# Kernel optimization log

Hardware: AMD Instinct MI355X
Metric: run time of the kernel (lower is better)

The kernel has to match this reference:

```python
import jax, jax.numpy as jnp
import numpy as np

B, L1, NUM_C, DIM_S, SIZE_M = 64, 199, 1000, 64, 50


def setup_inputs() -> dict:
    key = jax.random.key(0)
    ks = jax.random.split(key, 16)
    inp = {
        "cseqs": jax.random.randint(ks[0], (B, L1), 0, NUM_C),
        "rseqs": jax.random.randint(ks[1], (B, L1), 0, 2),
        "shft_cseqs": jax.random.randint(ks[2], (B, L1), 0, NUM_C),
        "shft_rseqs": jax.random.randint(ks[3], (B, L1), 0, 2),
        # learned parameters (linear weights stored as [in, out])
        "kemb": jax.random.normal(ks[4], (NUM_C, DIM_S)) * 0.05,
        "vemb": jax.random.normal(ks[5], (2 * NUM_C, DIM_S)) * 0.05,
        "Mk": jax.random.normal(ks[6], (SIZE_M, DIM_S)) * (2.0 / DIM_S) ** 0.5,
        "Mv0": jax.random.normal(ks[7], (SIZE_M, DIM_S)) * (2.0 / DIM_S) ** 0.5,
        "Wf": jax.random.normal(ks[8], (2 * DIM_S, DIM_S)) * 0.05,
        "bf": jnp.zeros((DIM_S,)),
        "We": jax.random.normal(ks[9], (DIM_S, DIM_S)) * 0.05,
        "be": jnp.zeros((DIM_S,)),
        "Wa": jax.random.normal(ks[10], (DIM_S, DIM_S)) * 0.05,
        "ba": jnp.zeros((DIM_S,)),
        "Wp": jax.random.normal(ks[11], (DIM_S, 1)) * 0.05,
        "bp": jnp.zeros((1,)),
    }
    return inp


def reference(cseqs, rseqs, shft_cseqs, shft_rseqs,
              kemb, vemb, Mk, Mv0, Wf, bf, We, be, Wa, ba, Wp, bp):
    # reconstruct full-length sequences: [B, L] with L = L1 + 1
    q = jnp.concatenate([cseqs[:, :1], shft_cseqs], axis=-1)
    r = jnp.concatenate([rseqs[:, :1], shft_rseqs], axis=-1)
    x = q + NUM_C * r

    k = kemb[q]                                  # [B, L, D]
    v = vemb[x]                                  # [B, L, D]

    w = jax.nn.softmax(k @ Mk.T, axis=-1)        # [B, L, M] correlation weights
    e = jax.nn.sigmoid(v @ We + be)              # [B, L, D] erase
    a = jnp.tanh(v @ Wa + ba)                    # [B, L, D] add

    def step(Mvt, inp):
        et, at, wt = inp                         # [B,D], [B,D], [B,M]
        Mv_prev = Mvt                            # memory BEFORE this update (used for read)
        Mvt = Mvt * (1.0 - wt[:, :, None] * et[:, None, :]) + wt[:, :, None] * at[:, None, :]
        return Mvt, Mv_prev

    Mv_init = jnp.broadcast_to(Mv0[None], (B, SIZE_M, DIM_S))
    _, Mv_prev = jax.lax.scan(
        step, Mv_init,
        (e.transpose(1, 0, 2), a.transpose(1, 0, 2), w.transpose(1, 0, 2)))
    Mv_prev = Mv_prev.transpose(1, 0, 2, 3)      # [B, L, M, D]

    read = jnp.einsum('blm,blmd->bld', w, Mv_prev)   # weighted read
    info = jnp.concatenate([read, k], axis=-1)       # [B, L, 2D]
    f = jnp.tanh(info @ Wf + bf)                     # dropout is identity in eval
    p = jax.nn.sigmoid((f @ Wp + bp).squeeze(-1))    # [B, L]
    return p
```

## Files before the change

kernel.cpp:

```cpp
#include <hip/hip_runtime.h>
#include <math.h>

#define B    64
#define L1   199
#define L    200
#define NC   1000
#define D    64
#define M    50
#define SEG  4
#define TS   50
#define WV   5
#define MPW  10
#define BLK  320

__global__ __launch_bounds__(64) void phase0(
    const float* __restrict__ kemb, const float* __restrict__ vemb,
    const float* __restrict__ Mk,
    const float* __restrict__ We, const float* __restrict__ be,
    const float* __restrict__ Wa, const float* __restrict__ ba,
    const float* __restrict__ Wf,
    float* __restrict__ wtab, float* __restrict__ etab,
    float* __restrict__ atab, float* __restrict__ ktab)
{
    __shared__ __align__(16) float lrow[4 * D];
    const int lane = threadIdx.x;
    const int bid  = blockIdx.x;

    if (bid < 250) {
        const int r0 = bid * 4;
        #pragma unroll
        for (int i = 0; i < 4; ++i)
            lrow[i * D + lane] = kemb[(size_t)(r0 + i) * D + lane];
        __syncthreads();

        float Mk_r[D];
        {
            const int mrow = (lane < M) ? lane : (M - 1);
            #pragma unroll
            for (int d = 0; d < D; d += 4) {
                const float4 t4 = *(const float4*)(Mk + mrow * D + d);
                Mk_r[d] = t4.x; Mk_r[d+1] = t4.y; Mk_r[d+2] = t4.z; Mk_r[d+3] = t4.w;
            }
        }
        #pragma unroll
        for (int i = 0; i < 4; ++i) {
            float c0 = 0.f, c1 = 0.f;
            #pragma unroll
            for (int d = 0; d < D; d += 4) {
                const float4 kb = *(const float4*)&lrow[i * D + d];
                c0 = fmaf(Mk_r[d],     kb.x, c0);
                c1 = fmaf(Mk_r[d + 1], kb.y, c1);
                c0 = fmaf(Mk_r[d + 2], kb.z, c0);
                c1 = fmaf(Mk_r[d + 3], kb.w, c1);
            }
            const float logit = (lane < M) ? (c0 + c1) : -INFINITY;
            float mx = logit;
            #pragma unroll
            for (int off = 32; off; off >>= 1) mx = fmaxf(mx, __shfl_xor(mx, off, 64));
            const float ex = expf(logit - mx);
            float sm = ex;
            #pragma unroll
            for (int off = 32; off; off >>= 1) sm += __shfl_xor(sm, off, 64);
            if (lane < M) wtab[(size_t)(r0 + i) * M + lane] = ex / sm;
        }
    } else if (bid < 1250) {
        const bool is_e = (bid < 750);
        const int  r0   = (is_e ? (bid - 250) : (bid - 750)) * 4;
        #pragma unroll
        for (int i = 0; i < 4; ++i)
            lrow[i * D + lane] = vemb[(size_t)(r0 + i) * D + lane];
        __syncthreads();

        const float* __restrict__ W   = is_e ? We : Wa;
        float*       __restrict__ dst = is_e ? etab : atab;
        float Wc[D];
        #pragma unroll
        for (int din = 0; din < D; ++din) Wc[din] = W[din * D + lane];
        const float br = is_e ? be[lane] : ba[lane];

        #pragma unroll
        for (int i = 0; i < 4; ++i) {
            float c0 = 0.f, c1 = 0.f;
            #pragma unroll
            for (int d = 0; d < D; d += 4) {
                const float4 vb = *(const float4*)&lrow[i * D + d];
                c0 = fmaf(Wc[d],     vb.x, c0);
                c1 = fmaf(Wc[d + 1], vb.y, c1);
                c0 = fmaf(Wc[d + 2], vb.z, c0);
                c1 = fmaf(Wc[d + 3], vb.w, c1);
            }
            const float acc = c0 + c1;
            const float r = is_e ? (1.f / (1.f + expf(-(acc + br))))
                                 : tanhf(acc + br);
            dst[(size_t)(r0 + i) * D + lane] = r;
        }
    } else {
        const int r0 = (bid - 1250) * 4;
        #pragma unroll
        for (int i = 0; i < 4; ++i)
            lrow[i * D + lane] = kemb[(size_t)(r0 + i) * D + lane];
        __syncthreads();

        float Wc[D];
        #pragma unroll
        for (int i = 0; i < D; ++i) Wc[i] = Wf[(size_t)(D + i) * D + lane];

        #pragma unroll
        for (int i = 0; i < 4; ++i) {
            float f1 = 0.f;
            #pragma unroll
            for (int d = 0; d < D; d += 4) {
                const float4 kb = *(const float4*)&lrow[i * D + d];
                f1 = fmaf(Wc[d],     kb.x, f1);
                f1 = fmaf(Wc[d + 1], kb.y, f1);
                f1 = fmaf(Wc[d + 2], kb.z, f1);
                f1 = fmaf(Wc[d + 3], kb.w, f1);
            }
            ktab[(size_t)(r0 + i) * D + lane] = f1;
        }
    }
}

__global__ __launch_bounds__(BLK, 1) void scan3(
    const int* __restrict__ cseqs, const int* __restrict__ rseqs,
    const int* __restrict__ shft_cseqs, const int* __restrict__ shft_rseqs,
    const float* __restrict__ Mv0,
    const float* __restrict__ wtab, const float* __restrict__ etab,
    const float* __restrict__ atab, const float* __restrict__ ktab,
    const float* __restrict__ Wf, const float* __restrict__ bf,
    const float* __restrict__ Wp, const float* __restrict__ bp,
    float* __restrict__ out)
{
    __shared__ __align__(16) float s_ea[2][TS][D];
    __shared__ __align__(16) float s_ww[WV][TS][12];
    __shared__ __align__(16) float s_part[WV][TS][D];
    __shared__ int s_q[L];
    __shared__ int s_x[L];

    const int tid  = threadIdx.x;
    const int lane = tid & 63;
    const int wv   = tid >> 6;
    const int blk  = blockIdx.x;
    const int b    = blk >> 2;
    const int s    = blk & 3;
    const int m0   = wv * MPW;

    if (tid < L) {
        const int t = tid;
        int q, r;
        if (t == 0) { q = cseqs[b * L1];              r = rseqs[b * L1]; }
        else        { q = shft_cseqs[b * L1 + t - 1]; r = shft_rseqs[b * L1 + t - 1]; }
        s_q[t] = q;
        s_x[t] = q + NC * r;
    }
    __syncthreads();

    float Mv[MPW];
    #pragma unroll
    for (int j = 0; j < MPW; ++j) Mv[j] = Mv0[(m0 + j) * D + lane];

    for (int ss = 0; ss <= s; ++ss) {
        const int tb = ss * TS;
        #pragma unroll
        for (int j = 0; j < MPW; ++j) {
            const int t = wv * MPW + j;
            const int x = s_x[tb + t];
            s_ea[0][t][lane] = etab[(size_t)x * D + lane];
            s_ea[1][t][lane] = atab[(size_t)x * D + lane];
        }
        if (lane < TS) {
            const int q = s_q[tb + lane];
            const float* __restrict__ wp_ = wtab + (size_t)q * M + m0;
            #pragma unroll
            for (int j = 0; j < MPW; ++j) s_ww[wv][lane][j] = wp_[j];
        }
        __syncthreads();

        if (ss < s) {
            for (int t = 0; t < TS; ++t) {
                const float ed = s_ea[0][t][lane];
                const float ad = s_ea[1][t][lane];
                float wl[MPW];
                *(float4*)&wl[0] = *(const float4*)&s_ww[wv][t][0];
                *(float4*)&wl[4] = *(const float4*)&s_ww[wv][t][4];
                wl[8] = s_ww[wv][t][8];
                wl[9] = s_ww[wv][t][9];
                #pragma unroll
                for (int j = 0; j < MPW; ++j) {
                    const float wm = wl[j];
                    const float we = wm * ed;
                    Mv[j] = fmaf(Mv[j], -we, fmaf(wm, ad, Mv[j]));
                }
            }
        } else {
            for (int t = 0; t < TS; ++t) {
                const float ed = s_ea[0][t][lane];
                const float ad = s_ea[1][t][lane];
                float wl[MPW];
                *(float4*)&wl[0] = *(const float4*)&s_ww[wv][t][0];
                *(float4*)&wl[4] = *(const float4*)&s_ww[wv][t][4];
                wl[8] = s_ww[wv][t][8];
                wl[9] = s_ww[wv][t][9];
                float r0a = 0.f, r1a = 0.f, r0b = 0.f, r1b = 0.f;
                #pragma unroll
                for (int j = 0; j < 5; ++j) {
                    const float wm = wl[j];
                    if (j & 1) r1a = fmaf(wm, Mv[j], r1a);
                    else       r0a = fmaf(wm, Mv[j], r0a);
                    const float we = wm * ed;
                    Mv[j] = fmaf(Mv[j], -we, fmaf(wm, ad, Mv[j]));
                }
                #pragma unroll
                for (int j = 5; j < 10; ++j) {
                    const float wm = wl[j];
                    if ((j - 5) & 1) r1b = fmaf(wm, Mv[j], r1b);
                    else             r0b = fmaf(wm, Mv[j], r0b);
                    const float we = wm * ed;
                    Mv[j] = fmaf(Mv[j], -we, fmaf(wm, ad, Mv[j]));
                }
                s_part[wv][t][lane] = (r0a + r1a) + (r0b + r1b);
            }
        }
        __syncthreads();
    }

    {
        float Wf_c[D];
        #pragma unroll
        for (int i = 0; i < D; ++i) Wf_c[i] = Wf[(size_t)i * D + lane];
        const float bf_r = bf[lane];
        const float wp_r = Wp[lane];
        const float bp_r = bp[0];
        const int t0 = s * TS;

        #pragma unroll
        for (int j = 0; j < MPW; ++j) {
            const int t = wv * MPW + j;
            const float rd = (((s_part[0][t][lane] + s_part[1][t][lane])
                              + s_part[2][t][lane]) + s_part[3][t][lane])
                              + s_part[4][t][lane];
            const float kt = ktab[(size_t)s_q[t0 + t] * D + lane];
            s_ea[0][t][lane] = rd;
            float f0 = 0.f;
            #pragma unroll
            for (int i = 0; i < D; i += 4) {
                const float4 rb = *(const float4*)&s_ea[0][t][i];
                f0 = fmaf(Wf_c[i],     rb.x, f0);
                f0 = fmaf(Wf_c[i + 1], rb.y, f0);
                f0 = fmaf(Wf_c[i + 2], rb.z, f0);
                f0 = fmaf(Wf_c[i + 3], rb.w, f0);
            }
            const float f = tanhf(f0 + kt + bf_r);
            float c = f * wp_r;
            #pragma unroll
            for (int off = 32; off; off >>= 1) c += __shfl_xor(c, off, 64);
            if (lane == 0) out[b * L + t0 + t] = 1.f / (1.f + expf(-(c + bp_r)));
        }
    }
}

extern "C" void kernel_launch(void* const* d_in, const int* in_sizes, int n_in,
                              void* d_out, int out_size, void* d_ws, size_t ws_size,
                              hipStream_t stream) {
    const int*   cseqs      = (const int*)d_in[0];
    const int*   rseqs      = (const int*)d_in[1];
    const int*   shft_cseqs = (const int*)d_in[2];
    const int*   shft_rseqs = (const int*)d_in[3];
    const float* kemb = (const float*)d_in[4];
    const float* vemb = (const float*)d_in[5];
    const float* Mk   = (const float*)d_in[6];
    const float* Mv0  = (const float*)d_in[7];
    const float* Wf   = (const float*)d_in[8];
    const float* bf   = (const float*)d_in[9];
    const float* We   = (const float*)d_in[10];
    const float* be   = (const float*)d_in[11];
    const float* Wa   = (const float*)d_in[12];
    const float* ba   = (const float*)d_in[13];
    const float* Wp   = (const float*)d_in[14];
    const float* bp   = (const float*)d_in[15];
    float* out = (float*)d_out;

    float* ws   = (float*)d_ws;
    float* wtab = ws;
    float* etab = wtab + (size_t)NC * M;
    float* atab = etab + (size_t)2 * NC * D;
    float* ktab = atab + (size_t)2 * NC * D;

    phase0<<<dim3(1500), dim3(64), 0, stream>>>(
        kemb, vemb, Mk, We, be, Wa, ba, Wf, wtab, etab, atab, ktab);
    scan3<<<dim3(B * SEG), dim3(BLK), 0, stream>>>(
        cseqs, rseqs, shft_cseqs, shft_rseqs, Mv0,
        wtab, etab, atab, ktab, Wf, bf, Wp, bp, out);
}
```

Measured before the change: 125.6 us.

## Double-buffer scan segment loads and process 8 rows per phase0 block

```diff
diff --git a/kernel.cpp b/kernel.cpp
--- a/kernel.cpp
+++ b/kernel.cpp
@@ -22,14 +22,14 @@
     float* __restrict__ wtab, float* __restrict__ etab,
     float* __restrict__ atab, float* __restrict__ ktab)
 {
-    __shared__ __align__(16) float lrow[4 * D];
+    __shared__ __align__(16) float lrow[8 * D];
     const int lane = threadIdx.x;
     const int bid  = blockIdx.x;
 
-    if (bid < 250) {
-        const int r0 = bid * 4;
-        #pragma unroll
-        for (int i = 0; i < 4; ++i)
+    if (bid < 125) {
+        const int r0 = bid * 8;
+        #pragma unroll
+        for (int i = 0; i < 8; ++i)
             lrow[i * D + lane] = kemb[(size_t)(r0 + i) * D + lane];
         __syncthreads();
 
@@ -43,7 +43,7 @@
             }
         }
         #pragma unroll
-        for (int i = 0; i < 4; ++i) {
+        for (int i = 0; i < 8; ++i) {
             float c0 = 0.f, c1 = 0.f;
             #pragma unroll
             for (int d = 0; d < D; d += 4) {
@@ -63,11 +63,11 @@
             for (int off = 32; off; off >>= 1) sm += __shfl_xor(sm, off, 64);
             if (lane < M) wtab[(size_t)(r0 + i) * M + lane] = ex / sm;
         }
-    } else if (bid < 1250) {
-        const bool is_e = (bid < 750);
-        const int  r0   = (is_e ? (bid - 250) : (bid - 750)) * 4;
-        #pragma unroll
-        for (int i = 0; i < 4; ++i)
+    } else if (bid < 625) {
+        const bool is_e = (bid < 375);
+        const int  r0   = (is_e ? (bid - 125) : (bid - 375)) * 8;
+        #pragma unroll
+        for (int i = 0; i < 8; ++i)
             lrow[i * D + lane] = vemb[(size_t)(r0 + i) * D + lane];
         __syncthreads();
 
@@ -79,7 +79,7 @@
         const float br = is_e ? be[lane] : ba[lane];
 
         #pragma unroll
-        for (int i = 0; i < 4; ++i) {
+        for (int i = 0; i < 8; ++i) {
             float c0 = 0.f, c1 = 0.f;
             #pragma unroll
             for (int d = 0; d < D; d += 4) {
@@ -95,9 +95,9 @@
             dst[(size_t)(r0 + i) * D + lane] = r;
         }
     } else {
-        const int r0 = (bid - 1250) * 4;
-        #pragma unroll
-        for (int i = 0; i < 4; ++i)
+        const int r0 = (bid - 625) * 8;
+        #pragma unroll
+        for (int i = 0; i < 8; ++i)
             lrow[i * D + lane] = kemb[(size_t)(r0 + i) * D + lane];
         __syncthreads();
 
@@ -106,7 +106,7 @@
         for (int i = 0; i < D; ++i) Wc[i] = Wf[(size_t)(D + i) * D + lane];
 
         #pragma unroll
-        for (int i = 0; i < 4; ++i) {
+        for (int i = 0; i < 8; ++i) {
             float f1 = 0.f;
             #pragma unroll
             for (int d = 0; d < D; d += 4) {
@@ -131,8 +131,8 @@
     const float* __restrict__ Wp, const float* __restrict__ bp,
     float* __restrict__ out)
 {
-    __shared__ __align__(16) float s_ea[2][TS][D];
-    __shared__ __align__(16) float s_ww[WV][TS][12];
+    __shared__ __align__(16) float s_ea[2][2][TS][D];
+    __shared__ __align__(16) float s_ww[2][WV][TS][12];
     __shared__ __align__(16) float s_part[WV][TS][D];
     __shared__ int s_q[L];
     __shared__ int s_x[L];
@@ -159,32 +159,51 @@
     #pragma unroll
     for (int j = 0; j < MPW; ++j) Mv[j] = Mv0[(m0 + j) * D + lane];
 
+    #pragma unroll
+    for (int j = 0; j < MPW; ++j) {
+        const int t = wv * MPW + j;
+        const int x = s_x[t];
+        s_ea[0][0][t][lane] = etab[(size_t)x * D + lane];
+        s_ea[0][1][t][lane] = atab[(size_t)x * D + lane];
+    }
+    if (lane < TS) {
+        const int q = s_q[lane];
+        const float* __restrict__ wp_ = wtab + (size_t)q * M + m0;
+        #pragma unroll
+        for (int j = 0; j < MPW; ++j) s_ww[0][wv][lane][j] = wp_[j];
+    }
+    __syncthreads();
+
+    int cur = 0;
     for (int ss = 0; ss <= s; ++ss) {
-        const int tb = ss * TS;
-        #pragma unroll
-        for (int j = 0; j < MPW; ++j) {
-            const int t = wv * MPW + j;
-            const int x = s_x[tb + t];
-            s_ea[0][t][lane] = etab[(size_t)x * D + lane];
-            s_ea[1][t][lane] = atab[(size_t)x * D + lane];
-        }
-        if (lane < TS) {
-            const int q = s_q[tb + lane];
-            const float* __restrict__ wp_ = wtab + (size_t)q * M + m0;
-            #pragma unroll
-            for (int j = 0; j < MPW; ++j) s_ww[wv][lane][j] = wp_[j];
-        }
-        __syncthreads();
+        const bool has_next = (ss < s);
+        float er_n[MPW], ar_n[MPW], wn[MPW];
+        if (has_next) {
+            const int tb2 = (ss + 1) * TS;
+            #pragma unroll
+            for (int j = 0; j < MPW; ++j) {
+                const int t = wv * MPW + j;
+                const int x = s_x[tb2 + t];
+                er_n[j] = etab[(size_t)x * D + lane];
+                ar_n[j] = atab[(size_t)x * D + lane];
+            }
+            if (lane < TS) {
+                const int q = s_q[tb2 + lane];
+                const float* __restrict__ wp_ = wtab + (size_t)q * M + m0;
+                #pragma unroll
+                for (int j = 0; j < MPW; ++j) wn[j] = wp_[j];
+            }
+        }
 
         if (ss < s) {
             for (int t = 0; t < TS; ++t) {
-                const float ed = s_ea[0][t][lane];
-                const float ad = s_ea[1][t][lane];
+                const float ed = s_ea[cur][0][t][lane];
+                const float ad = s_ea[cur][1][t][lane];
                 float wl[MPW];
-                *(float4*)&wl[0] = *(const float4*)&s_ww[wv][t][0];
-                *(float4*)&wl[4] = *(const float4*)&s_ww[wv][t][4];
-                wl[8] = s_ww[wv][t][8];
-                wl[9] = s_ww[wv][t][9];
+                *(float4*)&wl[0] = *(const float4*)&s_ww[cur][wv][t][0];
+                *(float4*)&wl[4] = *(const float4*)&s_ww[cur][wv][t][4];
+                wl[8] = s_ww[cur][wv][t][8];
+                wl[9] = s_ww[cur][wv][t][9];
                 #pragma unroll
                 for (int j = 0; j < MPW; ++j) {
                     const float wm = wl[j];
@@ -194,13 +213,13 @@
             }
         } else {
             for (int t = 0; t < TS; ++t) {
-                const float ed = s_ea[0][t][lane];
-                const float ad = s_ea[1][t][lane];
+                const float ed = s_ea[cur][0][t][lane];
+                const float ad = s_ea[cur][1][t][lane];
                 float wl[MPW];
-                *(float4*)&wl[0] = *(const float4*)&s_ww[wv][t][0];
-                *(float4*)&wl[4] = *(const float4*)&s_ww[wv][t][4];
-                wl[8] = s_ww[wv][t][8];
-                wl[9] = s_ww[wv][t][9];
+                *(float4*)&wl[0] = *(const float4*)&s_ww[cur][wv][t][0];
+                *(float4*)&wl[4] = *(const float4*)&s_ww[cur][wv][t][4];
+                wl[8] = s_ww[cur][wv][t][8];
+                wl[9] = s_ww[cur][wv][t][9];
                 float r0a = 0.f, r1a = 0.f, r0b = 0.f, r1b = 0.f;
                 #pragma unroll
                 for (int j = 0; j < 5; ++j) {
@@ -221,7 +240,22 @@
                 s_part[wv][t][lane] = (r0a + r1a) + (r0b + r1b);
             }
         }
+
+        if (has_next) {
+            const int nb = cur ^ 1;
+            #pragma unroll
+            for (int j = 0; j < MPW; ++j) {
+                const int t = wv * MPW + j;
+                s_ea[nb][0][t][lane] = er_n[j];
+                s_ea[nb][1][t][lane] = ar_n[j];
+            }
+            if (lane < TS) {
+                #pragma unroll
+                for (int j = 0; j < MPW; ++j) s_ww[nb][wv][lane][j] = wn[j];
+            }
+        }
         __syncthreads();
+        cur ^= 1;
     }
 
     {
@@ -240,11 +274,11 @@
                               + s_part[2][t][lane]) + s_part[3][t][lane])
                               + s_part[4][t][lane];
             const float kt = ktab[(size_t)s_q[t0 + t] * D + lane];
-            s_ea[0][t][lane] = rd;
+            s_ea[0][0][t][lane] = rd;
             float f0 = 0.f;
             #pragma unroll
             for (int i = 0; i < D; i += 4) {
-                const float4 rb = *(const float4*)&s_ea[0][t][i];
+                const float4 rb = *(const float4*)&s_ea[0][0][t][i];
                 f0 = fmaf(Wf_c[i],     rb.x, f0);
                 f0 = fmaf(Wf_c[i + 1], rb.y, f0);
                 f0 = fmaf(Wf_c[i + 2], rb.z, f0);
@@ -286,7 +320,7 @@
     float* atab = etab + (size_t)2 * NC * D;
     float* ktab = atab + (size_t)2 * NC * D;
 
-    phase0<<<dim3(1500), dim3(64), 0, stream>>>(
+    phase0<<<dim3(750), dim3(64), 0, stream>>>(
         kemb, vemb, Mk, We, be, Wa, ba, Wf, wtab, etab, atab, ktab);
     scan3<<<dim3(B * SEG), dim3(BLK), 0, stream>>>(
         cseqs, rseqs, shft_cseqs, shft_rseqs, Mv0,
```

Result: no change. 126.0 us (+0.4%).
